# Kernel optimization log

Hardware: AMD Instinct MI355X
Metric: run time of the kernel (lower is better)

Reference implementation:

```python
import jax, jax.numpy as jnp
import numpy as np

B, L, D_MODEL = 4, 2048, 1024
D_INNER = 2 * D_MODEL
D_STATE, DT_RANK = 16, 64
Q = 32768.0  # 2^15 dyadic denominator used by the block


def _find_power_of_2_scale(var, eps=1e-9):
    v = var + eps
    scale = jnp.ones_like(v)
    for t, s in [(4.0, 0.5), (16.0, 0.25), (64.0, 0.125), (256.0, 0.0625),
                 (1024.0, 0.03125), (4096.0, 0.015625), (16384.0, 0.0078125),
                 (65536.0, 0.00390625)]:
        scale = jnp.where(v >= t, s, scale)
    scale = jnp.where(v < 1.0, 1.0, scale)
    scale = jnp.where(v < 0.25, 2.0, scale)
    scale = jnp.where(v < 0.0625, 4.0, scale)
    return scale


def _sigmoid_algebraic(z):
    return 0.5 + 0.5 * z / (1.0 + jnp.abs(z))


def _rsqrt_newton(y, num_iters=3):
    y = jnp.clip(y, 1e-6, 1e6)
    r = jnp.where(y > 16.0, 0.125, 0.5)
    r = jnp.where(y > 64.0, 0.0625, r)
    r = jnp.where(y > 256.0, 0.03125, r)
    r = jnp.where(y < 4.0, 1.0, r)
    r = jnp.where(y < 1.0, 2.0, r)
    r = jnp.where(y < 0.25, 4.0, r)
    for _ in range(num_iters):
        r = jnp.clip(r * (1.5 - 0.5 * y * r * r), 1e-6, 1e3)
    return r


def _squareplus(x):
    y = jnp.clip(x * x + 4.0, 1e-6, 1e6)
    s = jnp.clip(y * _rsqrt_newton(y), 0.0, 1e3)
    return 0.5 * (x + s)


def bitshift_norm(x, gamma, step_size):
    xc = x - x.mean(axis=-1, keepdims=True)
    var = (xc * xc).mean(axis=-1, keepdims=True)
    inv_disc = _find_power_of_2_scale(var)
    inv_diff = jax.lax.rsqrt(var + 1e-6)
    inv = inv_diff + jax.lax.stop_gradient(inv_disc - inv_diff)  # LSQ-style STE
    return xc * inv * gamma * step_size


def bitlinear(x, W):
    # 1.58-bit BitLinear: ternary weight quantization with STE
    s = jnp.mean(jnp.abs(W)) + 1e-8
    Wq = jnp.clip(jnp.round(W / s), -1.0, 1.0) * s
    Wq = W + jax.lax.stop_gradient(Wq - W)
    return x @ Wq.T


def dyadic_scan(u, decay):
    # h[t] = decay[t] * h[t-1] + (1 - decay[t]) * u[t]  (convex combination)
    a = decay
    b = (1.0 - decay) * u
    def comb(c1, c2):
        a1, b1 = c1
        a2, b2 = c2
        return a1 * a2, a2 * b1 + b2
    _, h = jax.lax.associative_scan(comb, (a, b), axis=1)
    return h


def setup_inputs() -> dict:
    key = jax.random.key(0)
    ks = jax.random.split(key, 9)
    d = {}
    d["x"] = jax.random.normal(ks[0], (B, L, D_MODEL), dtype=jnp.float32)
    d["gamma"] = jnp.ones((D_MODEL,), jnp.float32)
    d["step_size"] = jnp.ones((1,), jnp.float32)
    d["W_in"] = jax.random.normal(ks[1], (2 * D_INNER, D_MODEL), jnp.float32) * (D_MODEL ** -0.5)
    d["conv_w"] = jax.random.normal(ks[2], (D_INNER, 1, 4), jnp.float32) * 0.5
    d["conv_b"] = jnp.zeros((D_INNER,), jnp.float32)
    d["W_x"] = jax.random.normal(ks[3], (DT_RANK + 2 * D_STATE, D_INNER), jnp.float32) * (D_INNER ** -0.5)
    d["W_dt"] = jax.random.normal(ks[4], (D_INNER, DT_RANK), jnp.float32) * (DT_RANK ** -0.5)
    d["b_dt"] = jax.random.normal(ks[5], (D_INNER,), jnp.float32) * 0.1
    d["W_out"] = jax.random.normal(ks[6], (D_MODEL, D_INNER), jnp.float32) * (D_INNER ** -0.5)
    return d


def reference(x, gamma, step_size, W_in, conv_w, conv_b, W_x, W_dt, b_dt, W_out):
    Bc, Lc, _ = x.shape
    residual = x
    xn = bitshift_norm(x, gamma, step_size)
    xz = bitlinear(xn, W_in)                      # [B, L, 2*d_inner]
    xc, z = jnp.split(xz, 2, axis=-1)
    # causal depthwise conv1d (kernel 4, torch padding=3, slice back to L)
    xt = xc.transpose(0, 2, 1)                    # [B, d_inner, L]
    y = jax.lax.conv_general_dilated(
        xt, conv_w, (1,), [(3, 3)],
        dimension_numbers=("NCH", "OIH", "NCH"),
        feature_group_count=D_INNER)
    xc = (y[..., :Lc] + conv_b[None, :, None]).transpose(0, 2, 1)
    xc = _squareplus(xc)                          # integer-only activation
    dbl = bitlinear(xc, W_x)                      # [B, L, dt_rank + 2*d_state]
    dt = bitlinear(dbl[..., :DT_RANK], W_dt) + b_dt  # [B, L, d_inner]
    decay_c = _sigmoid_algebraic(dt)
    # dyadic quantization of decay to k/2^15 with STE
    decay = decay_c + jax.lax.stop_gradient(jnp.round(decay_c * Q) / Q - decay_c)
    h = dyadic_scan(xc, decay)                    # [B, L, d_inner]
    y = h * _squareplus(z)
    return bitlinear(y, W_out) + residual
```

## Files before the change

### kernel.cpp

```cpp
#include <hip/hip_runtime.h>
#include <hip/hip_bf16.h>

#define B_ 4
#define L_ 2048
#define DM 1024
#define DI 2048
#define NR (B_ * L_)
#define DTR 64
#define NCHUNK 32
#define CHUNK 64
#define CCONV 64
#define KSLICE 8

typedef __attribute__((ext_vector_type(8))) short short8;
typedef __attribute__((ext_vector_type(4))) float floatx4;
typedef __attribute__((ext_vector_type(4))) int int4v;

static constexpr size_t OFF_SCAL = 0;
static constexpr size_t OFF_PART = 256;
static constexpr size_t OFF_XN   = 4608;
static constexpr size_t OFF_TIN  = OFF_XN   + (size_t)NR * DM * 2;
static constexpr size_t OFF_TX   = OFF_TIN  + (size_t)2 * DI * DM * 2;
static constexpr size_t OFF_TDT  = OFF_TX   + (size_t)DTR * DI * 2;
static constexpr size_t OFF_TOUT = OFF_TDT  + (size_t)DI * DTR * 2;
static constexpr size_t OFF_XC   = OFF_TOUT + (size_t)DM * DI * 2;
static constexpr size_t OFF_P2   = OFF_XC   + (size_t)NR * DI * 2;
static constexpr size_t OFF_ZSP  = OFF_XC   + (size_t)NR * DI * 4;
static constexpr size_t OFF_XACT = OFF_ZSP  + (size_t)NR * DI * 2;
static constexpr size_t OFF_DBL  = OFF_XACT + (size_t)NR * DI * 2;
static constexpr size_t OFF_DEC  = OFF_DBL  + (size_t)NR * DTR * 2;
static constexpr size_t OFF_CA   = OFF_DEC  + (size_t)NR * DI * 2;
static constexpr size_t OFF_CB   = OFF_CA   + (size_t)B_ * NCHUNK * DI * 4;
static constexpr size_t OFF_Y    = OFF_CB   + (size_t)B_ * NCHUNK * DI * 4;
static constexpr size_t OFF_SROW = OFF_Y    + (size_t)NR * DI * 2;

__device__ __forceinline__ void async16(const void* g, void* l) {
    __builtin_amdgcn_global_load_lds(
        (const __attribute__((address_space(1))) unsigned int*)g,
        (__attribute__((address_space(3))) unsigned int*)l, 16, 0, 0);
}

__device__ __forceinline__ float pow2scale(float var) {
    float v = var + 1e-9f;
    float s = 1.0f;
    if (v >= 4.0f)     s = 0.5f;
    if (v >= 16.0f)    s = 0.25f;
    if (v >= 64.0f)    s = 0.125f;
    if (v >= 256.0f)   s = 0.0625f;
    if (v >= 1024.0f)  s = 0.03125f;
    if (v >= 4096.0f)  s = 0.015625f;
    if (v >= 16384.0f) s = 0.0078125f;
    if (v >= 65536.0f) s = 0.00390625f;
    if (v < 1.0f)    s = 1.0f;
    if (v < 0.25f)   s = 2.0f;
    if (v < 0.0625f) s = 4.0f;
    return s;
}

__device__ __forceinline__ float squareplus_f(float x) {
    float y = fminf(fmaxf(x * x + 4.0f, 1e-6f), 1e6f);
    float r = (y > 16.0f) ? 0.125f : 0.5f;
    if (y > 64.0f)  r = 0.0625f;
    if (y > 256.0f) r = 0.03125f;
    if (y < 4.0f)   r = 1.0f;
    if (y < 1.0f)   r = 2.0f;
    if (y < 0.25f)  r = 4.0f;
#pragma unroll
    for (int i = 0; i < 3; ++i) {
        r = r * (1.5f - 0.5f * y * r * r);
        r = fminf(fmaxf(r, 1e-6f), 1e3f);
    }
    float s = fminf(fmaxf(y * r, 0.0f), 1e3f);
    return 0.5f * (x + s);
}

__device__ __forceinline__ float block_reduce_sum(float v) {
    __shared__ float sm[4];
#pragma unroll
    for (int o = 32; o > 0; o >>= 1) v += __shfl_down(v, o, 64);
    int w = threadIdx.x >> 6;
    __syncthreads();
    if ((threadIdx.x & 63) == 0) sm[w] = v;
    __syncthreads();
    return (sm[0] + sm[1]) + (sm[2] + sm[3]);
}

__device__ __forceinline__ float block_reduce_max(float v) {
    __shared__ float smx[4];
#pragma unroll
    for (int o = 32; o > 0; o >>= 1) v = fmaxf(v, __shfl_down(v, o, 64));
    int w = threadIdx.x >> 6;
    __syncthreads();
    if ((threadIdx.x & 63) == 0) smx[w] = v;
    __syncthreads();
    return fmaxf(fmaxf(smx[0], smx[1]), fmaxf(smx[2], smx[3]));
}

__global__ __launch_bounds__(256) void k_abs_all(const float* __restrict__ W0,
                                                 const float* __restrict__ W1,
                                                 const float* __restrict__ W2,
                                                 const float* __restrict__ W3,
                                                 float* __restrict__ part) {
    const int w = blockIdx.y;
    const float* W = (w == 0) ? W0 : (w == 1) ? W1 : (w == 2) ? W2 : W3;
    const int n4 = ((w == 0) ? 2 * DI * DM : (w == 1) ? 96 * DI : (w == 2) ? DI * DTR : DM * DI) / 4;
    const float4* W4 = (const float4*)W;
    float s = 0.f;
    for (int i = blockIdx.x * 256 + threadIdx.x; i < n4; i += 256 * 256) {
        float4 v = W4[i];
        s += fabsf(v.x) + fabsf(v.y) + fabsf(v.z) + fabsf(v.w);
    }
    float t = block_reduce_sum(s);
    if (threadIdx.x == 0) part[w * 256 + blockIdx.x] = t;
}

__global__ __launch_bounds__(256) void k_finalize(const float* __restrict__ part,
                                                  float* __restrict__ scal) {
    const float counts[4] = {(float)(2 * DI * DM), (float)(96 * DI),
                             (float)(DI * DTR), (float)(DM * DI)};
    for (int w = 0; w < 4; ++w) {
        float s = block_reduce_sum(part[w * 256 + threadIdx.x]);
        if (threadIdx.x == 0) scal[w] = s / counts[w] + 1e-8f;
    }
}

__global__ __launch_bounds__(256) void k_quant_all(
    const float* __restrict__ W0, const float* __restrict__ W1,
    const float* __restrict__ W2, const float* __restrict__ W3,
    const float* __restrict__ scal,
    signed char* __restrict__ T0, __hip_bfloat16* __restrict__ T1,
    __hip_bfloat16* __restrict__ T2, __hip_bfloat16* __restrict__ T3) {
    int b = blockIdx.x;
    if (b < 4096) {
        int i = b * 1024 + threadIdx.x * 4;
        float inv = 1.0f / scal[0];
        float4 v = *(const float4*)(W0 + i);
        int q0 = (int)fmaxf(-1.0f, fminf(1.0f, rintf(v.x * inv)));
        int q1 = (int)fmaxf(-1.0f, fminf(1.0f, rintf(v.y * inv)));
        int q2 = (int)fmaxf(-1.0f, fminf(1.0f, rintf(v.z * inv)));
        int q3 = (int)fmaxf(-1.0f, fminf(1.0f, rintf(v.w * inv)));
        unsigned int packed = (q0 & 255) | ((q1 & 255) << 8) | ((q2 & 255) << 16) | ((q3 & 255) << 24);
        *reinterpret_cast<unsigned int*>(&T0[i]) = packed;
        return;
    }
    const float* W; const float* sp; __hip_bfloat16* T; int off;
    if (b < 4224)      { W = W1; sp = scal + 1; T = T1; off = b - 4096; }
    else if (b < 4352) { W = W2; sp = scal + 2; T = T2; off = b - 4224; }
    else               { W = W3; sp = scal + 3; T = T3; off = b - 4352; }
    int i = off * 1024 + threadIdx.x * 4;
    float inv = 1.0f / (*sp);
    float4 v = *(const float4*)(W + i);
    __hip_bfloat16 t[4];
    t[0] = __float2bfloat16(fmaxf(-1.0f, fminf(1.0f, rintf(v.x * inv))));
    t[1] = __float2bfloat16(fmaxf(-1.0f, fminf(1.0f, rintf(v.y * inv))));
    t[2] = __float2bfloat16(fmaxf(-1.0f, fminf(1.0f, rintf(v.z * inv))));
    t[3] = __float2bfloat16(fmaxf(-1.0f, fminf(1.0f, rintf(v.w * inv))));
    *reinterpret_cast<uint2*>(&T[i]) = *reinterpret_cast<uint2*>(t);
}

__global__ __launch_bounds__(256) void k_norm(const float* __restrict__ x,
                                              const float* __restrict__ gamma,
                                              const float* __restrict__ step,
                                              signed char* __restrict__ xn8,
                                              float* __restrict__ srow) {
    int row = blockIdx.x;
    int tid = threadIdx.x;
    float4 v4 = ((const float4*)(x + (size_t)row * DM))[tid];
    float s = (v4.x + v4.y) + (v4.z + v4.w);
    float mean = block_reduce_sum(s) * (1.0f / DM);
    float d0 = v4.x - mean, d1 = v4.y - mean, d2 = v4.z - mean, d3 = v4.w - mean;
    float vv = d0 * d0 + d1 * d1 + d2 * d2 + d3 * d3;
    float var = block_reduce_sum(vv) * (1.0f / DM);
    float sc = pow2scale(var) * step[0];
    float4 g = ((const float4*)gamma)[tid];
    float w0 = d0 * sc * g.x, w1 = d1 * sc * g.y, w2 = d2 * sc * g.z, w3 = d3 * sc * g.w;
    float am = fmaxf(fmaxf(fabsf(w0), fabsf(w1)), fmaxf(fabsf(w2), fabsf(w3)));
    am = block_reduce_max(am);
    float sr = (am > 0.f) ? am * (1.0f / 127.0f) : 1.0f;
    float inv = 1.0f / sr;
    if (tid == 0) srow[row] = sr;
    int q0 = (int)rintf(w0 * inv), q1 = (int)rintf(w1 * inv);
    int q2 = (int)rintf(w2 * inv), q3 = (int)rintf(w3 * inv);
    unsigned int packed = (q0 & 255) | ((q1 & 255) << 8) | ((q2 & 255) << 16) | ((q3 & 255) << 24);
    ((unsigned int*)xn8)[row * 256 + tid] = packed;
}

__global__ __launch_bounds__(256) void k_gemm1_i8(
    const signed char* __restrict__ A, const signed char* __restrict__ Bw,
    const float* __restrict__ s_ptr, const float* __restrict__ srow,
    __hip_bfloat16* __restrict__ o_xc, __hip_bfloat16* __restrict__ o_z) {
    constexpr int BM = 128, BN = 128, BKB = 64;
    constexpr int FM = 4, FN = 4;
    constexpr int RA = 2, RB = 2, KEEP = RA + RB;
    constexpr int K = DM, NT = K / 64;
    __shared__ __align__(16) signed char lA[3][BM * BKB];
    __shared__ __align__(16) signed char lB[3][BN * BKB];
    const int tid = threadIdx.x;
    const int lane = tid & 63, wid = tid >> 6;
    const int wm = (wid >> 1) * 64;
    const int wn = (wid & 1) * 64;
    const int r16 = lane & 15, quad = lane >> 4;

    int nx = gridDim.x;
    int bx = blockIdx.x, by = blockIdx.y;
    {
        int bid = by * nx + bx;
        int xcd = bid & 7, idx = bid >> 3;
        int npx = nx >> 3;
        bx = xcd * npx + (idx % npx);
        by = idx / npx;
    }
    const int m0 = by * BM, n0 = bx * BN;

    int4v acc[FM][FN] = {};

#pragma unroll
    for (int p = 0; p < 2; ++p) {
#pragma unroll
        for (int r = 0; r < RA; ++r) {
            int idx = r * 256 + tid;
            int row = idx >> 2, kc = (idx & 3) << 4;
            async16(&A[(size_t)(m0 + row) * K + p * 64 + kc], &lA[p][idx * 16]);
        }
#pragma unroll
        for (int r = 0; r < RB; ++r) {
            int idx = r * 256 + tid;
            int row = idx >> 2, kc = (idx & 3) << 4;
            async16(&Bw[(size_t)(n0 + row) * K + p * 64 + kc], &lB[p][idx * 16]);
        }
    }

    for (int t = 0; t < NT; ++t) {
        if (t > 0) __builtin_amdgcn_s_barrier();
        if (t + 2 < NT) {
            const int k2 = (t + 2) * 64;
            const int nb = (t + 2) % 3;
#pragma unroll
            for (int r = 0; r < RA; ++r) {
                int idx = r * 256 + tid;
                int row = idx >> 2, kc = (idx & 3) << 4;
                async16(&A[(size_t)(m0 + row) * K + k2 + kc], &lA[nb][idx * 16]);
            }
#pragma unroll
            for (int r = 0; r < RB; ++r) {
                int idx = r * 256 + tid;
                int row = idx >> 2, kc = (idx & 3) << 4;
                async16(&Bw[(size_t)(n0 + row) * K + k2 + kc], &lB[nb][idx * 16]);
            }
            __builtin_amdgcn_s_waitcnt(0x0F70 | (2 * KEEP));
        } else if (t + 1 < NT) {
            __builtin_amdgcn_s_waitcnt(0x0F70 | KEEP);
        } else {
            __builtin_amdgcn_s_waitcnt(0x0F70);
        }
        __builtin_amdgcn_s_barrier();

        const int cb = t % 3;
        int4v af[FM], bfv[FN];
#pragma unroll
        for (int i = 0; i < FM; ++i)
            af[i] = *reinterpret_cast<const int4v*>(&lA[cb][(wm + i * 16 + r16) * BKB + quad * 16]);
#pragma unroll
        for (int j = 0; j < FN; ++j)
            bfv[j] = *reinterpret_cast<const int4v*>(&lB[cb][(wn + j * 16 + r16) * BKB + quad * 16]);
#pragma unroll
        for (int i = 0; i < FM; ++i)
#pragma unroll
            for (int j = 0; j < FN; ++j)
                acc[i][j] = __builtin_amdgcn_mfma_i32_16x16x64_i8(af[i], bfv[j], acc[i][j], 0, 0, 0);
    }

    const float sW = *s_ptr;
#pragma unroll
    for (int i = 0; i < FM; ++i) {
#pragma unroll
        for (int j = 0; j < FN; ++j) {
#pragma unroll
            for (int r = 0; r < 4; ++r) {
                int gr = m0 + wm + i * 16 + quad * 4 + r;
                int gc = n0 + wn + j * 16 + r16;
                float v = (float)acc[i][j][r] * sW * srow[gr];
                if (gc < DI) o_xc[(size_t)gr * DI + gc] = __float2bfloat16(v);
                else         o_z[(size_t)gr * DI + (gc - DI)] = __float2bfloat16(v);
            }
        }
    }
}

template <int BM, int BN, int WR, int WC, int MODE>
__global__ __launch_bounds__(256) void k_gemm(
    const __hip_bfloat16* __restrict__ A, const __hip_bfloat16* __restrict__ Bw,
    int M, int N, int K, int lda, int ldb, const float* __restrict__ s_ptr,
    float* __restrict__ o_f32, __hip_bfloat16* __restrict__ o_bf16,
    unsigned short* __restrict__ o_u16,
    const float* __restrict__ bias, const float* __restrict__ resid) {
    constexpr int BK = 32;
    constexpr int FM = BM / (WR * 16), FN = BN / (WC * 16);
    constexpr int RA = (BM * BK) / (256 * 8);
    constexpr int RB = (BN * BK) / (256 * 8);
    constexpr int KEEP = RA + RB;
    __shared__ __align__(16) short lA[3][BM * BK];
    __shared__ __align__(16) short lB[3][BN * BK];
    const int tid = threadIdx.x;
    const int lane = tid & 63, wid = tid >> 6;
    const int wm = (wid / WC) * (BM / WR);
    const int wn = (wid % WC) * (BN / WC);
    const int r16 = lane & 15, quad = lane >> 4;

    if (MODE == 4) {
        A  += (size_t)blockIdx.z * K;
        Bw += (size_t)blockIdx.z * K;
        o_f32 += (size_t)blockIdx.z * M * N;
    }

    int nx = gridDim.x;
    int bx = blockIdx.x, by = blockIdx.y;
    if ((nx & 7) == 0 && nx >= 8) {
        int bid = by * nx + bx;
        int xcd = bid & 7, idx = bid >> 3;
        int npx = nx >> 3;
        bx = xcd * npx + (idx % npx);
        by = idx / npx;
    }
    const int m0 = by * BM, n0 = bx * BN;

    floatx4 acc[FM][FN] = {};
    const int NT = K / BK;

#pragma unroll
    for (int r = 0; r < RA; ++r) {
        int idx = r * 256 + tid;
        int row = idx >> 2, kc = (idx & 3) << 3;
        async16(&A[(size_t)(m0 + row) * lda + kc], &lA[0][idx * 8]);
    }
#pragma unroll
    for (int r = 0; r < RB; ++r) {
        int idx = r * 256 + tid;
        int row = idx >> 2, kc = (idx & 3) << 3;
        async16(&Bw[(size_t)(n0 + row) * ldb + kc], &lB[0][idx * 8]);
    }
    if (NT > 1) {
#pragma unroll
        for (int r = 0; r < RA; ++r) {
            int idx = r * 256 + tid;
            int row = idx >> 2, kc = (idx & 3) << 3;
            async16(&A[(size_t)(m0 + row) * lda + BK + kc], &lA[1][idx * 8]);
        }
#pragma unroll
        for (int r = 0; r < RB; ++r) {
            int idx = r * 256 + tid;
            int row = idx >> 2, kc = (idx & 3) << 3;
            async16(&Bw[(size_t)(n0 + row) * ldb + BK + kc], &lB[1][idx * 8]);
        }
    }

    for (int t = 0; t < NT; ++t) {
        if (t > 0) __builtin_amdgcn_s_barrier();
        if (t + 2 < NT) {
            const int k2 = (t + 2) * BK;
            const int nb = (t + 2) % 3;
#pragma unroll
            for (int r = 0; r < RA; ++r) {
                int idx = r * 256 + tid;
                int row = idx >> 2, kc = (idx & 3) << 3;
                async16(&A[(size_t)(m0 + row) * lda + k2 + kc], &lA[nb][idx * 8]);
            }
#pragma unroll
            for (int r = 0; r < RB; ++r) {
                int idx = r * 256 + tid;
                int row = idx >> 2, kc = (idx & 3) << 3;
                async16(&Bw[(size_t)(n0 + row) * ldb + k2 + kc], &lB[nb][idx * 8]);
            }
            __builtin_amdgcn_s_waitcnt(0x0F70 | (2 * KEEP));
        } else if (t + 1 < NT) {
            __builtin_amdgcn_s_waitcnt(0x0F70 | KEEP);
        } else {
            __builtin_amdgcn_s_waitcnt(0x0F70);
        }
        __builtin_amdgcn_s_barrier();

        const int cb = t % 3;
        short8 af[FM], bfv[FN];
#pragma unroll
        for (int i = 0; i < FM; ++i)
            af[i] = *reinterpret_cast<const short8*>(&lA[cb][(wm + i * 16 + r16) * BK + quad * 8]);
#pragma unroll
        for (int j = 0; j < FN; ++j)
            bfv[j] = *reinterpret_cast<const short8*>(&lB[cb][(wn + j * 16 + r16) * BK + quad * 8]);
#pragma unroll
        for (int i = 0; i < FM; ++i)
#pragma unroll
            for (int j = 0; j < FN; ++j)
                acc[i][j] = __builtin_amdgcn_mfma_f32_16x16x32_bf16(af[i], bfv[j], acc[i][j], 0, 0, 0);
    }

    const float s = (MODE == 4) ? 1.0f : *s_ptr;
#pragma unroll
    for (int i = 0; i < FM; ++i) {
#pragma unroll
        for (int j = 0; j < FN; ++j) {
#pragma unroll
            for (int r = 0; r < 4; ++r) {
                int gr = m0 + wm + i * 16 + quad * 4 + r;
                int gc = n0 + wn + j * 16 + r16;
                float v = acc[i][j][r] * s;
                if (MODE == 1) {
                    o_bf16[(size_t)gr * N + gc] = __float2bfloat16(v);
                } else if (MODE == 2) {
                    float dt = v + bias[gc];
                    float dc = 0.5f + 0.5f * dt / (1.0f + fabsf(dt));
                    o_u16[(size_t)gr * N + gc] = (unsigned short)rintf(dc * 32768.0f);
                } else if (MODE == 3) {
                    o_f32[(size_t)gr * N + gc] = v + resid[(size_t)gr * N + gc];
                } else {
                    o_f32[(size_t)gr * N + gc] = v;
                }
            }
        }
    }
}

__global__ __launch_bounds__(256) void k_red(const float* __restrict__ part,
                                             const float* __restrict__ s_ptr,
                                             __hip_bfloat16* __restrict__ dbl) {
    int i = blockIdx.x * 256 + threadIdx.x;
    float s = *s_ptr;
    float acc = 0.f;
#pragma unroll
    for (int z = 0; z < KSLICE; ++z) acc += part[(size_t)z * NR * DTR + i];
    dbl[i] = __float2bfloat16(acc * s);
}

__global__ __launch_bounds__(256) void k_conv(const __hip_bfloat16* __restrict__ xc,
                                              const float* __restrict__ cw,
                                              const float* __restrict__ cb,
                                              __hip_bfloat16* __restrict__ xact) {
    int c = blockIdx.x * 256 + threadIdx.x;
    int t0 = blockIdx.y * CCONV;
    int b = blockIdx.z;
    float w0 = cw[c * 4 + 0], w1 = cw[c * 4 + 1], w2 = cw[c * 4 + 2], w3 = cw[c * 4 + 3];
    float bias = cb[c];
    const __hip_bfloat16* base = xc + (size_t)b * L_ * DI + c;
    float x3 = (t0 - 3 >= 0) ? __bfloat162float(base[(size_t)(t0 - 3) * DI]) : 0.f;
    float x2 = (t0 - 2 >= 0) ? __bfloat162float(base[(size_t)(t0 - 2) * DI]) : 0.f;
    float x1 = (t0 - 1 >= 0) ? __bfloat162float(base[(size_t)(t0 - 1) * DI]) : 0.f;
    for (int t = t0; t < t0 + CCONV; ++t) {
        float xt = __bfloat162float(base[(size_t)t * DI]);
        float y = x3 * w0 + x2 * w1 + x1 * w2 + xt * w3 + bias;
        xact[((size_t)(b * L_ + t)) * DI + c] = __float2bfloat16(squareplus_f(y));
        x3 = x2; x2 = x1; x1 = xt;
    }
}

__global__ __launch_bounds__(256) void k_scan1(const unsigned short* __restrict__ dk,
                                               const __hip_bfloat16* __restrict__ u,
                                               float* __restrict__ cA, float* __restrict__ cB) {
    int c = blockIdx.x * 256 + threadIdx.x;
    int j = blockIdx.y, b = blockIdx.z;
    size_t base = ((size_t)b * L_ + (size_t)j * CHUNK) * DI + c;
    float Ac = 1.f, Bc = 0.f;
    for (int t = 0; t < CHUNK; ++t) {
        float a = dk[base + (size_t)t * DI] * (1.0f / 32768.0f);
        float uv = __bfloat162float(u[base + (size_t)t * DI]);
        Bc = a * Bc + (1.f - a) * uv;
        Ac *= a;
    }
    size_t o = ((size_t)(b * NCHUNK + j)) * DI + c;
    cA[o] = Ac;
    cB[o] = Bc;
}

__global__ __launch_bounds__(256) void k_scan3(const unsigned short* __restrict__ dk,
                                               const __hip_bfloat16* __restrict__ u,
                                               const __hip_bfloat16* __restrict__ zraw,
                                               const float* __restrict__ cA,
                                               const float* __restrict__ cB,
                                               __hip_bfloat16* __restrict__ y) {
    int c = blockIdx.x * 256 + threadIdx.x;
    int j = blockIdx.y, b = blockIdx.z;
    float h = 0.f;
    for (int jj = 0; jj < j; ++jj) {
        size_t o = ((size_t)(b * NCHUNK + jj)) * DI + c;
        h = cA[o] * h + cB[o];
    }
    size_t base = ((size_t)b * L_ + (size_t)j * CHUNK) * DI + c;
    for (int t = 0; t < CHUNK; ++t) {
        float a = dk[base + (size_t)t * DI] * (1.0f / 32768.0f);
        float uv = __bfloat162float(u[base + (size_t)t * DI]);
        h = a * h + (1.f - a) * uv;
        float zv = squareplus_f(__bfloat162float(zraw[base + (size_t)t * DI]));
        y[base + (size_t)t * DI] = __float2bfloat16(h * zv);
    }
}

extern "C" void kernel_launch(void* const* d_in, const int* in_sizes, int n_in,
                              void* d_out, int out_size, void* d_ws, size_t ws_size,
                              hipStream_t stream) {
    const float* x      = (const float*)d_in[0];
    const float* gamma  = (const float*)d_in[1];
    const float* step   = (const float*)d_in[2];
    const float* W_in   = (const float*)d_in[3];
    const float* conv_w = (const float*)d_in[4];
    const float* conv_b = (const float*)d_in[5];
    const float* W_x    = (const float*)d_in[6];
    const float* W_dt   = (const float*)d_in[7];
    const float* b_dt   = (const float*)d_in[8];
    const float* W_out  = (const float*)d_in[9];

    char* ws = (char*)d_ws;
    float*          scal = (float*)(ws + OFF_SCAL);
    float*          part = (float*)(ws + OFF_PART);
    signed char*    xn8  = (signed char*)(ws + OFF_XN);
    signed char*    Tin8 = (signed char*)(ws + OFF_TIN);
    __hip_bfloat16* Tx   = (__hip_bfloat16*)(ws + OFF_TX);
    __hip_bfloat16* Tdt  = (__hip_bfloat16*)(ws + OFF_TDT);
    __hip_bfloat16* Tout = (__hip_bfloat16*)(ws + OFF_TOUT);
    __hip_bfloat16* xcb  = (__hip_bfloat16*)(ws + OFF_XC);
    float*          p2   = (float*)(ws + OFF_P2);
    __hip_bfloat16* zraw = (__hip_bfloat16*)(ws + OFF_ZSP);
    __hip_bfloat16* xact = (__hip_bfloat16*)(ws + OFF_XACT);
    __hip_bfloat16* dbl  = (__hip_bfloat16*)(ws + OFF_DBL);
    unsigned short* dec  = (unsigned short*)(ws + OFF_DEC);
    float*          cA   = (float*)(ws + OFF_CA);
    float*          cB   = (float*)(ws + OFF_CB);
    __hip_bfloat16* yb   = (__hip_bfloat16*)(ws + OFF_Y);
    float*          srow = (float*)(ws + OFF_SROW);
    float*          out  = (float*)d_out;

    k_abs_all<<<dim3(256, 4), 256, 0, stream>>>(W_in, W_x, W_dt, W_out, part);
    k_finalize<<<1, 256, 0, stream>>>(part, scal);
    k_quant_all<<<6400, 256, 0, stream>>>(W_in, W_x, W_dt, W_out, scal, Tin8, Tx, Tdt, Tout);

    k_norm<<<NR, 256, 0, stream>>>(x, gamma, step, xn8, srow);

    k_gemm1_i8<<<dim3((2 * DI) / 128, NR / 128), 256, 0, stream>>>(
        xn8, Tin8, scal + 0, srow, xcb, zraw);

    k_conv<<<dim3(DI / 256, L_ / CCONV, B_), 256, 0, stream>>>(xcb, conv_w, conv_b, xact);

    k_gemm<64, 64, 2, 2, 4><<<dim3(1, NR / 64, KSLICE), 256, 0, stream>>>(
        xact, Tx, NR, DTR, DI / KSLICE, DI, DI, nullptr, p2, nullptr, nullptr, nullptr, nullptr);
    k_red<<<(NR * DTR) / 256, 256, 0, stream>>>(p2, scal + 1, dbl);

    k_gemm<64, 128, 2, 2, 2><<<dim3(DI / 128, NR / 64), 256, 0, stream>>>(
        dbl, Tdt, NR, DI, DTR, DTR, DTR, scal + 2, nullptr, nullptr, dec, b_dt, nullptr);

    k_scan1<<<dim3(DI / 256, NCHUNK, B_), 256, 0, stream>>>(dec, xact, cA, cB);
    k_scan3<<<dim3(DI / 256, NCHUNK, B_), 256, 0, stream>>>(dec, xact, zraw, cA, cB, yb);

    k_gemm<64, 128, 2, 2, 3><<<dim3(DM / 128, NR / 64), 256, 0, stream>>>(
        yb, Tout, NR, DM, DI, DI, DI, scal + 3, out, nullptr, nullptr, nullptr, x);

    (void)in_sizes; (void)n_in; (void)out_size; (void)ws_size;
}
```

Measured before the change: 343.6 us.

## Quantize scan output to int8 per row and run output projection with int8 MFMA

The scan kernel now tracks a per-row absmax of y through wave reductions and atomicMax, a new kernel quantizes y to int8 with that scale, and the final projection runs on a new int8 MFMA GEMM against ternary int8 W_out, with the residual fused into its epilogue. W_out is now quantized to int8 instead of bf16. This targets the bandwidth and compute of the bf16 output GEMM. The cost is an extra quantization pass, a memset, per-timestep atomics in the scan, and an activation-rounding error that the reference does not have. The XCD-aware block remapping in the generic GEMM is also removed.

After: 356.1 us. +3.6%, slower.

```diff
diff --git a/kernel.cpp b/kernel.cpp
--- a/kernel.cpp
+++ b/kernel.cpp
@@ -33,6 +33,7 @@
 static constexpr size_t OFF_CB   = OFF_CA   + (size_t)B_ * NCHUNK * DI * 4;
 static constexpr size_t OFF_Y    = OFF_CB   + (size_t)B_ * NCHUNK * DI * 4;
 static constexpr size_t OFF_SROW = OFF_Y    + (size_t)NR * DI * 2;
+static constexpr size_t OFF_PMAX = OFF_SROW + (size_t)NR * 4;
 
 __device__ __forceinline__ void async16(const void* g, void* l) {
     __builtin_amdgcn_global_load_lds(
@@ -129,24 +130,26 @@
     const float* __restrict__ W2, const float* __restrict__ W3,
     const float* __restrict__ scal,
     signed char* __restrict__ T0, __hip_bfloat16* __restrict__ T1,
-    __hip_bfloat16* __restrict__ T2, __hip_bfloat16* __restrict__ T3) {
+    __hip_bfloat16* __restrict__ T2, signed char* __restrict__ T3) {
     int b = blockIdx.x;
-    if (b < 4096) {
-        int i = b * 1024 + threadIdx.x * 4;
-        float inv = 1.0f / scal[0];
-        float4 v = *(const float4*)(W0 + i);
+    if (b < 4096 || b >= 4352) {
+        const float* W; const float* sp; signed char* T; int off;
+        if (b < 4096) { W = W0; sp = scal + 0; T = T0; off = b; }
+        else          { W = W3; sp = scal + 3; T = T3; off = b - 4352; }
+        int i = off * 1024 + threadIdx.x * 4;
+        float inv = 1.0f / (*sp);
+        float4 v = *(const float4*)(W + i);
         int q0 = (int)fmaxf(-1.0f, fminf(1.0f, rintf(v.x * inv)));
         int q1 = (int)fmaxf(-1.0f, fminf(1.0f, rintf(v.y * inv)));
         int q2 = (int)fmaxf(-1.0f, fminf(1.0f, rintf(v.z * inv)));
         int q3 = (int)fmaxf(-1.0f, fminf(1.0f, rintf(v.w * inv)));
         unsigned int packed = (q0 & 255) | ((q1 & 255) << 8) | ((q2 & 255) << 16) | ((q3 & 255) << 24);
-        *reinterpret_cast<unsigned int*>(&T0[i]) = packed;
+        *reinterpret_cast<unsigned int*>(&T[i]) = packed;
         return;
     }
     const float* W; const float* sp; __hip_bfloat16* T; int off;
-    if (b < 4224)      { W = W1; sp = scal + 1; T = T1; off = b - 4096; }
-    else if (b < 4352) { W = W2; sp = scal + 2; T = T2; off = b - 4224; }
-    else               { W = W3; sp = scal + 3; T = T3; off = b - 4352; }
+    if (b < 4224) { W = W1; sp = scal + 1; T = T1; off = b - 4096; }
+    else          { W = W2; sp = scal + 2; T = T2; off = b - 4224; }
     int i = off * 1024 + threadIdx.x * 4;
     float inv = 1.0f / (*sp);
     float4 v = *(const float4*)(W + i);
@@ -287,6 +290,98 @@
     }
 }
 
+__global__ __launch_bounds__(256) void k_gemm4_i8(
+    const signed char* __restrict__ A, const signed char* __restrict__ Bw,
+    const float* __restrict__ s_ptr, const unsigned int* __restrict__ pmax,
+    const float* __restrict__ resid, float* __restrict__ out) {
+    constexpr int BM = 64, BN = 128, BKB = 64;
+    constexpr int FM = 2, FN = 4;
+    constexpr int RA = 1, RB = 2, KEEP = RA + RB;
+    constexpr int K = DI, NT = K / 64;
+    __shared__ __align__(16) signed char lA[3][BM * BKB];
+    __shared__ __align__(16) signed char lB[3][BN * BKB];
+    const int tid = threadIdx.x;
+    const int lane = tid & 63, wid = tid >> 6;
+    const int wm = (wid >> 1) * 32;
+    const int wn = (wid & 1) * 64;
+    const int r16 = lane & 15, quad = lane >> 4;
+
+    const int m0 = blockIdx.y * BM, n0 = blockIdx.x * BN;
+
+    int4v acc[FM][FN] = {};
+
+#pragma unroll
+    for (int p = 0; p < 2; ++p) {
+#pragma unroll
+        for (int r = 0; r < RA; ++r) {
+            int idx = r * 256 + tid;
+            int row = idx >> 2, kc = (idx & 3) << 4;
+            async16(&A[(size_t)(m0 + row) * K + p * 64 + kc], &lA[p][idx * 16]);
+        }
+#pragma unroll
+        for (int r = 0; r < RB; ++r) {
+            int idx = r * 256 + tid;
+            int row = idx >> 2, kc = (idx & 3) << 4;
+            async16(&Bw[(size_t)(n0 + row) * K + p * 64 + kc], &lB[p][idx * 16]);
+        }
+    }
+
+    for (int t = 0; t < NT; ++t) {
+        if (t > 0) __builtin_amdgcn_s_barrier();
+        if (t + 2 < NT) {
+            const int k2 = (t + 2) * 64;
+            const int nb = (t + 2) % 3;
+#pragma unroll
+            for (int r = 0; r < RA; ++r) {
+                int idx = r * 256 + tid;
+                int row = idx >> 2, kc = (idx & 3) << 4;
+                async16(&A[(size_t)(m0 + row) * K + k2 + kc], &lA[nb][idx * 16]);
+            }
+#pragma unroll
+            for (int r = 0; r < RB; ++r) {
+                int idx = r * 256 + tid;
+                int row = idx >> 2, kc = (idx & 3) << 4;
+                async16(&Bw[(size_t)(n0 + row) * K + k2 + kc], &lB[nb][idx * 16]);
+            }
+            __builtin_amdgcn_s_waitcnt(0x0F70 | (2 * KEEP));
+        } else if (t + 1 < NT) {
+            __builtin_amdgcn_s_waitcnt(0x0F70 | KEEP);
+        } else {
+            __builtin_amdgcn_s_waitcnt(0x0F70);
+        }
+        __builtin_amdgcn_s_barrier();
+
+        const int cb = t % 3;
+        int4v af[FM], bfv[FN];
+#pragma unroll
+        for (int i = 0; i < FM; ++i)
+            af[i] = *reinterpret_cast<const int4v*>(&lA[cb][(wm + i * 16 + r16) * BKB + quad * 16]);
+#pragma unroll
+        for (int j = 0; j < FN; ++j)
+            bfv[j] = *reinterpret_cast<const int4v*>(&lB[cb][(wn + j * 16 + r16) * BKB + quad * 16]);
+#pragma unroll
+        for (int i = 0; i < FM; ++i)
+#pragma unroll
+            for (int j = 0; j < FN; ++j)
+                acc[i][j] = __builtin_amdgcn_mfma_i32_16x16x64_i8(af[i], bfv[j], acc[i][j], 0, 0, 0);
+    }
+
+    const float sW = *s_ptr;
+#pragma unroll
+    for (int i = 0; i < FM; ++i) {
+#pragma unroll
+        for (int r = 0; r < 4; ++r) {
+            int gr = m0 + wm + i * 16 + quad * 4 + r;
+            float sy = __uint_as_float(pmax[gr]) * (1.0f / 127.0f) * sW;
+#pragma unroll
+            for (int j = 0; j < FN; ++j) {
+                int gc = n0 + wn + j * 16 + r16;
+                out[(size_t)gr * DM + gc] = (float)acc[i][j][r] * sy + resid[(size_t)gr * DM + gc];
+            }
+        }
+    }
+}
+
 template <int BM, int BN, int WR, int WC, int MODE>
 __global__ __launch_bounds__(256) void k_gemm(
     const __hip_bfloat16* __restrict__ A, const __hip_bfloat16* __restrict__ Bw,
@@ -313,16 +408,7 @@
         o_f32 += (size_t)blockIdx.z * M * N;
     }
 
-    int nx = gridDim.x;
-    int bx = blockIdx.x, by = blockIdx.y;
-    if ((nx & 7) == 0 && nx >= 8) {
-        int bid = by * nx + bx;
-        int xcd = bid & 7, idx = bid >> 3;
-        int npx = nx >> 3;
-        bx = xcd * npx + (idx % npx);
-        by = idx / npx;
-    }
-    const int m0 = by * BM, n0 = bx * BN;
+    const int m0 = blockIdx.y * BM, n0 = blockIdx.x * BN;
 
     floatx4 acc[FM][FN] = {};
     const int NT = K / BK;
@@ -404,20 +490,17 @@
                 int gr = m0 + wm + i * 16 + quad * 4 + r;
                 int gc = n0 + wn + j * 16 + r16;
                 float v = acc[i][j][r] * s;
-                if (MODE == 1) {
-                    o_bf16[(size_t)gr * N + gc] = __float2bfloat16(v);
-                } else if (MODE == 2) {
+                if (MODE == 2) {
                     float dt = v + bias[gc];
                     float dc = 0.5f + 0.5f * dt / (1.0f + fabsf(dt));
                     o_u16[(size_t)gr * N + gc] = (unsigned short)rintf(dc * 32768.0f);
-                } else if (MODE == 3) {
-                    o_f32[(size_t)gr * N + gc] = v + resid[(size_t)gr * N + gc];
                 } else {
                     o_f32[(size_t)gr * N + gc] = v;
                 }
             }
         }
     }
+    (void)o_bf16; (void)resid;
 }
 
 __global__ __launch_bounds__(256) void k_red(const float* __restrict__ part,
@@ -475,7 +558,8 @@
                                                const __hip_bfloat16* __restrict__ zraw,
                                                const float* __restrict__ cA,
                                                const float* __restrict__ cB,
-                                               __hip_bfloat16* __restrict__ y) {
+                                               __hip_bfloat16* __restrict__ y,
+                                               unsigned int* __restrict__ pmax) {
     int c = blockIdx.x * 256 + threadIdx.x;
     int j = blockIdx.y, b = blockIdx.z;
     float h = 0.f;
@@ -484,13 +568,41 @@
         h = cA[o] * h + cB[o];
     }
     size_t base = ((size_t)b * L_ + (size_t)j * CHUNK) * DI + c;
+    const int lane = threadIdx.x & 63;
     for (int t = 0; t < CHUNK; ++t) {
         float a = dk[base + (size_t)t * DI] * (1.0f / 32768.0f);
         float uv = __bfloat162float(u[base + (size_t)t * DI]);
         h = a * h + (1.f - a) * uv;
         float zv = squareplus_f(__bfloat162float(zraw[base + (size_t)t * DI]));
-        y[base + (size_t)t * DI] = __float2bfloat16(h * zv);
-    }
+        float yv = h * zv;
+        y[base + (size_t)t * DI] = __float2bfloat16(yv);
+        float m = fabsf(yv);
+#pragma unroll
+        for (int o = 32; o > 0; o >>= 1) m = fmaxf(m, __shfl_down(m, o, 64));
+        if (lane == 0)
+            atomicMax(&pmax[(size_t)b * L_ + (size_t)j * CHUNK + t], __float_as_uint(m));
+    }
+}
+
+__global__ __launch_bounds__(256) void k_qy(const __hip_bfloat16* __restrict__ y,
+                                            const unsigned int* __restrict__ pmax,
+                                            signed char* __restrict__ y8) {
+    int g = blockIdx.x * 256 + threadIdx.x;
+    int i = g * 4;
+    int row = i >> 11;
+    float m = __uint_as_float(pmax[row]);
+    float inv = (m > 0.f) ? 127.0f / m : 0.f;
+    uint2 u = ((const uint2*)y)[g];
+    float f0 = __uint_as_float(u.x << 16);
+    float f1 = __uint_as_float(u.x & 0xffff0000u);
+    float f2 = __uint_as_float(u.y << 16);
+    float f3 = __uint_as_float(u.y & 0xffff0000u);
+    int q0 = (int)rintf(fminf(fmaxf(f0 * inv, -127.f), 127.f));
+    int q1 = (int)rintf(fminf(fmaxf(f1 * inv, -127.f), 127.f));
+    int q2 = (int)rintf(fminf(fmaxf(f2 * inv, -127.f), 127.f));
+    int q3 = (int)rintf(fminf(fmaxf(f3 * inv, -127.f), 127.f));
+    unsigned int packed = (q0 & 255) | ((q1 & 255) << 8) | ((q2 & 255) << 16) | ((q3 & 255) << 24);
+    *reinterpret_cast<unsigned int*>(&y8[i]) = packed;
 }
 
 extern "C" void kernel_launch(void* const* d_in, const int* in_sizes, int n_in,
@@ -514,9 +626,10 @@
     signed char*    Tin8 = (signed char*)(ws + OFF_TIN);
     __hip_bfloat16* Tx   = (__hip_bfloat16*)(ws + OFF_TX);
     __hip_bfloat16* Tdt  = (__hip_bfloat16*)(ws + OFF_TDT);
-    __hip_bfloat16* Tout = (__hip_bfloat16*)(ws + OFF_TOUT);
+    signed char*    Tout8= (signed char*)(ws + OFF_TOUT);
     __hip_bfloat16* xcb  = (__hip_bfloat16*)(ws + OFF_XC);
     float*          p2   = (float*)(ws + OFF_P2);
+    signed char*    y8   = (signed char*)(ws + OFF_P2);
     __hip_bfloat16* zraw = (__hip_bfloat16*)(ws + OFF_ZSP);
     __hip_bfloat16* xact = (__hip_bfloat16*)(ws + OFF_XACT);
     __hip_bfloat16* dbl  = (__hip_bfloat16*)(ws + OFF_DBL);
@@ -525,11 +638,12 @@
     float*          cB   = (float*)(ws + OFF_CB);
     __hip_bfloat16* yb   = (__hip_bfloat16*)(ws + OFF_Y);
     float*          srow = (float*)(ws + OFF_SROW);
+    unsigned int*   pmax = (unsigned int*)(ws + OFF_PMAX);
     float*          out  = (float*)d_out;
 
     k_abs_all<<<dim3(256, 4), 256, 0, stream>>>(W_in, W_x, W_dt, W_out, part);
     k_finalize<<<1, 256, 0, stream>>>(part, scal);
-    k_quant_all<<<6400, 256, 0, stream>>>(W_in, W_x, W_dt, W_out, scal, Tin8, Tx, Tdt, Tout);
+    k_quant_all<<<6400, 256, 0, stream>>>(W_in, W_x, W_dt, W_out, scal, Tin8, Tx, Tdt, Tout8);
 
     k_norm<<<NR, 256, 0, stream>>>(x, gamma, step, xn8, srow);
 
@@ -546,10 +660,12 @@
         dbl, Tdt, NR, DI, DTR, DTR, DTR, scal + 2, nullptr, nullptr, dec, b_dt, nullptr);
 
     k_scan1<<<dim3(DI / 256, NCHUNK, B_), 256, 0, stream>>>(dec, xact, cA, cB);
-    k_scan3<<<dim3(DI / 256, NCHUNK, B_), 256, 0, stream>>>(dec, xact, zraw, cA, cB, yb);
-
-    k_gemm<64, 128, 2, 2, 3><<<dim3(DM / 128, NR / 64), 256, 0, stream>>>(
-        yb, Tout, NR, DM, DI, DI, DI, scal + 3, out, nullptr, nullptr, nullptr, x);
+    hipMemsetAsync(pmax, 0, (size_t)NR * 4, stream);
+    k_scan3<<<dim3(DI / 256, NCHUNK, B_), 256, 0, stream>>>(dec, xact, zraw, cA, cB, yb, pmax);
+    k_qy<<<(NR * DI) / 1024, 256, 0, stream>>>(yb, pmax, y8);
+
+    k_gemm4_i8<<<dim3(DM / 128, NR / 64), 256, 0, stream>>>(
+        y8, Tout8, scal + 3, pmax, x, out);
 
     (void)in_sizes; (void)n_in; (void)out_size; (void)ws_size;
 }
```
